# Optimization experiments

Hardware: AMD Instinct MI355X
Metric: run time of the kernel (lower is better)

The kernel has to match this reference:

```python
import jax, jax.numpy as jnp
import numpy as np

N, E = 30000, 480000
D_IN, D_HID = 128, 256
NODE_CLS, EDGE_CLS, POLAR = 5, 2, 6
EPS = 1e-5

def layer_norm(x, g, b):
    mu = jnp.mean(x, axis=-1, keepdims=True)
    var = jnp.mean((x - mu) ** 2, axis=-1, keepdims=True)
    return g * (x - mu) / jnp.sqrt(var + EPS) + b

def sage_pool(h, src, dst, Wp, bp, Ws, bs, Wn, n_nodes):
    # DGL SAGEConv aggregator_type='pool': m = relu(fc_pool(h_src)); max over in-edges
    m = jax.nn.relu(h @ Wp + bp)              # [N, d_in]
    agg = jax.ops.segment_max(m[src], dst, num_segments=n_nodes)  # [N, d_in], -inf if no in-edges
    deg = jax.ops.segment_sum(jnp.ones((src.shape[0],), jnp.float32), dst, num_segments=n_nodes)
    h_neigh = jnp.where(deg[:, None] > 0, agg, 0.0)
    out = h @ Ws + bs + h_neigh @ Wn          # fc_self + fc_neigh
    return jax.nn.relu(out)                   # activation=F.relu

def setup_inputs() -> dict:
    key = jax.random.key(0)
    ks = jax.random.split(key, 24)
    p = lambda k, shape, fan: jax.random.normal(k, shape, jnp.float32) / np.sqrt(fan)
    return {
        "h": jax.random.normal(ks[0], (N, D_IN), jnp.float32),
        "efeat": jax.random.normal(ks[1], (E, POLAR), jnp.float32),
        "src": jax.random.randint(ks[2], (E,), 0, N, jnp.int32),
        "dst": jax.random.randint(ks[3], (E,), 0, N, jnp.int32),
        # encoder SAGEConv(128->256)
        "enc_Wpool": p(ks[4], (D_IN, D_IN), D_IN), "enc_bpool": jnp.zeros((D_IN,), jnp.float32),
        "enc_Wself": p(ks[5], (D_IN, D_HID), D_IN), "enc_bself": jnp.zeros((D_HID,), jnp.float32),
        "enc_Wneigh": p(ks[6], (D_IN, D_HID), D_IN),
        # node_pred: Linear(256,5) + LayerNorm(5)
        "np_W": p(ks[7], (D_HID, NODE_CLS), D_HID), "np_b": jnp.zeros((NODE_CLS,), jnp.float32),
        "np_g": jnp.ones((NODE_CLS,), jnp.float32), "np_beta": jnp.zeros((NODE_CLS,), jnp.float32),
        # edge predictor: Linear(528,256) + LN(256) + Linear(256,2)
        "ep_W1": p(ks[8], (2 * D_HID + 2 * NODE_CLS + POLAR, D_HID), 2 * D_HID + 16),
        "ep_b1": jnp.zeros((D_HID,), jnp.float32),
        "ep_g": jnp.ones((D_HID,), jnp.float32), "ep_beta": jnp.zeros((D_HID,), jnp.float32),
        "ep_W2": p(ks[9], (D_HID, EDGE_CLS), D_HID), "ep_b2": jnp.zeros((EDGE_CLS,), jnp.float32),
        # decoder SAGEConv(256->128)
        "dec_Wpool": p(ks[10], (D_HID, D_HID), D_HID), "dec_bpool": jnp.zeros((D_HID,), jnp.float32),
        "dec_Wself": p(ks[11], (D_HID, D_IN), D_HID), "dec_bself": jnp.zeros((D_IN,), jnp.float32),
        "dec_Wneigh": p(ks[12], (D_HID, D_IN), D_HID),
    }

def reference(h, efeat, src, dst,
              enc_Wpool, enc_bpool, enc_Wself, enc_bself, enc_Wneigh,
              np_W, np_b, np_g, np_beta,
              ep_W1, ep_b1, ep_g, ep_beta, ep_W2, ep_b2,
              dec_Wpool, dec_bpool, dec_Wself, dec_bself, dec_Wneigh):
    # encoder (drop_rate == 0 path)
    h1 = sage_pool(h, src, dst, enc_Wpool, enc_bpool, enc_Wself, enc_bself, enc_Wneigh, N)
    # node head
    node_pred = layer_norm(h1 @ np_W + np_b, np_g, np_beta)  # [N, 5]
    # edge head: gather-concat-MLP per edge
    cls_sm = jax.nn.softmax(node_pred, axis=1)               # softmax once, gather per edge
    x = jnp.concatenate([h1[src], cls_sm[src], efeat, h1[dst], cls_sm[dst]], axis=1)  # [E, 528]
    x = jax.nn.relu(layer_norm(x @ ep_W1 + ep_b1, ep_g, ep_beta))
    edges_pred = x @ ep_W2 + ep_b2                           # dropout is identity in eval
    # decoder (uses original graph, input h1)
    h2 = sage_pool(h1, src, dst, dec_Wpool, dec_bpool, dec_Wself, dec_bself, dec_Wneigh, N)
    return (node_pred, edges_pred, h2)
```

## Files before the change

### kernel.cpp

```cpp
#include <hip/hip_runtime.h>

typedef unsigned short u16;
typedef unsigned int u32;
typedef __bf16 bf16_t;
typedef bf16_t bf16x8 __attribute__((ext_vector_type(8)));
typedef float f32x4 __attribute__((ext_vector_type(4)));

#define N_NODES 30000
#define N_EDGES 480000

static __device__ __forceinline__ float b2f(u16 u) {
  return __uint_as_float(((u32)u) << 16);
}
static __device__ __forceinline__ float b2f_lo(u32 w) {
  return __uint_as_float(w << 16);
}
static __device__ __forceinline__ float b2f_hi(u32 w) {
  return __uint_as_float(w & 0xffff0000u);
}
static __device__ __forceinline__ u16 f2b(float f) {
  u32 x = __float_as_uint(f);
  u32 r = (x + 0x7fffu + ((x >> 16) & 1u)) >> 16;
  return (u16)r;
}

__global__ __launch_bounds__(256) void init_sniff_deg(const u16* __restrict__ h,
                                                      int* __restrict__ flag,
                                                      int* __restrict__ deg) {
  int i = blockIdx.x * 256 + threadIdx.x;
  if (i < N_NODES) deg[i] = 0;
  if (blockIdx.x == 0) {
    int t = threadIdx.x;
    int bad = 0;
#pragma unroll
    for (int j = 0; j < 4; j++) {
      u32 e = ((u32)h[t * 4 + j] >> 7) & 0xFFu;
      if (e >= 0x8Eu) bad = 1;
    }
    int r = __syncthreads_or(bad);
    if (t == 0) *flag = r ? 1 : 0;
  }
}

__global__ __launch_bounds__(256) void conv_arr4(const void* __restrict__ src,
                                                 u16* __restrict__ dst, int n4,
                                                 const int* __restrict__ flag) {
  int i = blockIdx.x * 256 + threadIdx.x;
  if (i >= n4) return;
  if (*flag) {
    float4 f = ((const float4*)src)[i];
    uint2 o;
    o.x = (u32)f2b(f.x) | ((u32)f2b(f.y) << 16);
    o.y = (u32)f2b(f.z) | ((u32)f2b(f.w) << 16);
    ((uint2*)dst)[i] = o;
  } else {
    ((uint2*)dst)[i] = ((const uint2*)src)[i];
  }
}

struct ConvDesc { const void* s; u16* d; int n; int off; };
struct ConvTab { ConvDesc e[20]; int total; };

__global__ __launch_bounds__(256) void conv_params(ConvTab tab, const int* __restrict__ flag) {
  int i = blockIdx.x * 256 + threadIdx.x;
  if (i >= tab.total) return;
  int f = *flag;
#pragma unroll 1
  for (int a = 0; a < 20; a++) {
    int j = i - tab.e[a].off;
    if (j >= 0 && j < tab.e[a].n) {
      if (f) tab.e[a].d[j] = f2b(((const float*)tab.e[a].s)[j]);
      else tab.e[a].d[j] = ((const u16*)tab.e[a].s)[j];
      return;
    }
  }
}

__global__ __launch_bounds__(256) void deg_count(const int* __restrict__ dst,
                                                 int* __restrict__ deg, int nE) {
  int e = blockIdx.x * 256 + threadIdx.x;
  if (e < nE) atomicAdd(&deg[dst[e]], 1);
}

__global__ __launch_bounds__(1024) void scan_off(const int* __restrict__ deg,
                                                 int* __restrict__ off,
                                                 int* __restrict__ cursor, int n) {
  __shared__ int carry;
  __shared__ int wsum[16];
  int t = threadIdx.x, lane = t & 63, wv = t >> 6;
  if (t == 0) { carry = 0; off[0] = 0; }
  __syncthreads();
  for (int base = 0; base < n; base += 1024) {
    int v = (base + t < n) ? deg[base + t] : 0;
    int x = v;
#pragma unroll
    for (int d = 1; d < 64; d <<= 1) {
      int y = __shfl_up(x, d, 64);
      if (lane >= d) x += y;
    }
    if (lane == 63) wsum[wv] = x;
    __syncthreads();
    int wadd = 0;
    for (int w = 0; w < wv; w++) wadd += wsum[w];
    int incl = x + wadd + carry;
    if (base + t < n) { off[base + t + 1] = incl; cursor[base + t] = incl - v; }
    __syncthreads();
    if (t == 1023) carry = incl;
    __syncthreads();
  }
}

__global__ __launch_bounds__(256) void fill_csr(const int* __restrict__ src,
                                                const int* __restrict__ dst,
                                                int* __restrict__ cursor,
                                                int* __restrict__ esrc, int nE) {
  int e = blockIdx.x * 256 + threadIdx.x;
  if (e >= nE) return;
  int p = atomicAdd(&cursor[dst[e]], 1);
  esrc[p] = src[e];
}

__global__ __launch_bounds__(256) void agg128(const u16* __restrict__ m,
                                              const int* __restrict__ esrc,
                                              const int* __restrict__ off,
                                              u16* __restrict__ out) {
  int wv = threadIdx.x >> 6, lane = threadIdx.x & 63;
  int n = blockIdx.x * 4 + wv;
  if (n >= N_NODES) return;
  int s0 = off[n], s1 = off[n + 1];
  u32 a0 = 0, a1 = 0;
  int i = s0;
  for (; i + 3 < s1; i += 4) {
    int e0 = esrc[i], e1 = esrc[i + 1], e2 = esrc[i + 2], e3 = esrc[i + 3];
    u32 r0 = *(const u32*)(m + (size_t)e0 * 128 + lane * 2);
    u32 r1 = *(const u32*)(m + (size_t)e1 * 128 + lane * 2);
    u32 r2 = *(const u32*)(m + (size_t)e2 * 128 + lane * 2);
    u32 r3 = *(const u32*)(m + (size_t)e3 * 128 + lane * 2);
    a0 = max(a0, r0 & 0xffffu); a1 = max(a1, r0 >> 16);
    a0 = max(a0, r1 & 0xffffu); a1 = max(a1, r1 >> 16);
    a0 = max(a0, r2 & 0xffffu); a1 = max(a1, r2 >> 16);
    a0 = max(a0, r3 & 0xffffu); a1 = max(a1, r3 >> 16);
  }
  for (; i < s1; i++) {
    u32 ra = *(const u32*)(m + (size_t)esrc[i] * 128 + lane * 2);
    a0 = max(a0, ra & 0xffffu); a1 = max(a1, ra >> 16);
  }
  *(u32*)(out + (size_t)n * 128 + lane * 2) = a0 | (a1 << 16);
}

__global__ __launch_bounds__(256) void agg256(const u16* __restrict__ m,
                                              const int* __restrict__ esrc,
                                              const int* __restrict__ off,
                                              u16* __restrict__ out) {
  int wv = threadIdx.x >> 6, lane = threadIdx.x & 63;
  int n = blockIdx.x * 4 + wv;
  if (n >= N_NODES) return;
  int s0 = off[n], s1 = off[n + 1];
  u32 a0 = 0, a1 = 0, a2 = 0, a3 = 0;
  int i = s0;
  for (; i + 3 < s1; i += 4) {
    int e0 = esrc[i], e1 = esrc[i + 1], e2 = esrc[i + 2], e3 = esrc[i + 3];
    uint2 r0 = *(const uint2*)(m + (size_t)e0 * 256 + lane * 4);
    uint2 r1 = *(const uint2*)(m + (size_t)e1 * 256 + lane * 4);
    uint2 r2 = *(const uint2*)(m + (size_t)e2 * 256 + lane * 4);
    uint2 r3 = *(const uint2*)(m + (size_t)e3 * 256 + lane * 4);
    a0 = max(a0, r0.x & 0xffffu); a1 = max(a1, r0.x >> 16);
    a2 = max(a2, r0.y & 0xffffu); a3 = max(a3, r0.y >> 16);
    a0 = max(a0, r1.x & 0xffffu); a1 = max(a1, r1.x >> 16);
    a2 = max(a2, r1.y & 0xffffu); a3 = max(a3, r1.y >> 16);
    a0 = max(a0, r2.x & 0xffffu); a1 = max(a1, r2.x >> 16);
    a2 = max(a2, r2.y & 0xffffu); a3 = max(a3, r2.y >> 16);
    a0 = max(a0, r3.x & 0xffffu); a1 = max(a1, r3.x >> 16);
    a2 = max(a2, r3.y & 0xffffu); a3 = max(a3, r3.y >> 16);
  }
  for (; i < s1; i++) {
    uint2 ra = *(const uint2*)(m + (size_t)esrc[i] * 256 + lane * 4);
    a0 = max(a0, ra.x & 0xffffu); a1 = max(a1, ra.x >> 16);
    a2 = max(a2, ra.y & 0xffffu); a3 = max(a3, ra.y >> 16);
  }
  uint2 w;
  w.x = a0 | (a1 << 16);
  w.y = a2 | (a3 << 16);
  *(uint2*)(out + (size_t)n * 256 + lane * 4) = w;
}

__global__ __launch_bounds__(256) void prep_weights(
    const u16* __restrict__ encWp, const u16* __restrict__ encWs, const u16* __restrict__ encWn,
    const u16* __restrict__ decWp, const u16* __restrict__ decWs, const u16* __restrict__ decWn,
    const u16* __restrict__ epW1, const u16* __restrict__ epb1,
    u16* __restrict__ wt_encpool, u16* __restrict__ wt_enc,
    u16* __restrict__ wt_decpool, u16* __restrict__ wt_dec,
    u16* __restrict__ wt_UV, u16* __restrict__ b512, float* __restrict__ swsum) {
  int b = blockIdx.x;
  const int t = threadIdx.x;
  if (b < 64) {
    int idx = b * 256 + t; int k = idx >> 7, n = idx & 127;
    wt_encpool[n * 128 + k] = encWp[k * 128 + n]; return;
  }
  b -= 64;
  if (b < 128) {
    int idx = b * 256 + t; int k = idx >> 8, n = idx & 255;
    wt_enc[n * 256 + k] = encWs[k * 256 + n]; return;
  }
  b -= 128;
  if (b < 128) {
    int idx = b * 256 + t; int k = idx >> 8, n = idx & 255;
    wt_enc[n * 256 + 128 + k] = encWn[k * 256 + n]; return;
  }
  b -= 128;
  if (b < 256) {
    int idx = b * 256 + t; int k = idx >> 8, n = idx & 255;
    wt_decpool[n * 256 + k] = decWp[k * 256 + n]; return;
  }
  b -= 256;
  if (b < 128) {
    int idx = b * 256 + t; int k = idx >> 7, n = idx & 127;
    wt_dec[n * 512 + k] = decWs[k * 128 + n]; return;
  }
  b -= 128;
  if (b < 128) {
    int idx = b * 256 + t; int k = idx >> 7, n = idx & 127;
    wt_dec[n * 512 + 256 + k] = decWn[k * 128 + n]; return;
  }
  b -= 128;
  if (b < 512) {
    int n = b, n2 = n & 255, base = (n >= 256) ? 267 : 0;
    for (int kp = t; kp < 288; kp += 256) {
      u16 v = (kp < 261) ? epW1[(size_t)(base + kp) * 256 + n2] : (u16)0;
      wt_UV[(size_t)n * 288 + kp] = v;
    }
    return;
  }
  b -= 512;
  if (b < 2) {
    int i = b * 256 + t;
    b512[i] = (i < 256) ? epb1[i] : (u16)0; return;
  }
  int k = t >> 5, l32 = t & 31;
  if (k < 6) {
    uint4 v = *(const uint4*)(epW1 + (size_t)(261 + k) * 256 + l32 * 8);
    float s = b2f_lo(v.x) + b2f_hi(v.x) + b2f_lo(v.y) + b2f_hi(v.y) +
              b2f_lo(v.z) + b2f_hi(v.z) + b2f_lo(v.w) + b2f_hi(v.w);
#pragma unroll
    for (int m = 1; m < 32; m <<= 1) s += __shfl_xor(s, m, 64);
    if (l32 == 0) swsum[k] = s;
  }
}

__global__ __launch_bounds__(256) void gemm_mfma(
    const u16* __restrict__ A0, const u16* __restrict__ A1, int K0, int K1,
    const u16* __restrict__ Bt, const u16* __restrict__ bias, int do_relu,
    u16* __restrict__ C, float* __restrict__ Cf, const int* __restrict__ flag,
    int M, int Nld) {
  __shared__ __align__(16) u16 As[128 * 40];
  __shared__ __align__(16) u16 Bs[128 * 40];
  const int t = threadIdx.x;
  const int lane = t & 63, wv = t >> 6;
  const int wm = wv & 1, wn = wv >> 1;
  const int r = lane & 15, q = lane >> 4;
  const int bm = blockIdx.x, bn = blockIdx.y;
  const int Ktot = K0 + K1;
  const bool usef = (Cf != nullptr) && (*flag != 0);

  f32x4 acc[4][4];
#pragma unroll
  for (int i = 0; i < 4; i++)
#pragma unroll
    for (int j = 0; j < 4; j++) acc[i][j] = (f32x4){0.f, 0.f, 0.f, 0.f};

  for (int kc = 0; kc < Ktot; kc += 32) {
#pragma unroll
    for (int h = 0; h < 2; h++) {
      int idx = t + h * 256;
      int rr = idx >> 2, qq = idx & 3;
      int rowg = bm * 128 + rr;
      uint4 av = make_uint4(0, 0, 0, 0);
      if (rowg < M) {
        const u16* p = (kc < K0) ? (A0 + (size_t)rowg * K0 + kc)
                                 : (A1 + (size_t)rowg * K1 + (kc - K0));
        av = *(const uint4*)(p + qq * 8);
      }
      *(uint4*)&As[rr * 40 + qq * 8] = av;
      int ng = bn * 128 + rr;
      uint4 bv = *(const uint4*)(Bt + (size_t)ng * Ktot + kc + qq * 8);
      *(uint4*)&Bs[rr * 40 + qq * 8] = bv;
    }
    __syncthreads();
    bf16x8 af[4], bfm[4];
#pragma unroll
    for (int mi = 0; mi < 4; mi++)
      af[mi] = *(const bf16x8*)&As[(wm * 64 + mi * 16 + r) * 40 + q * 8];
#pragma unroll
    for (int ni = 0; ni < 4; ni++)
      bfm[ni] = *(const bf16x8*)&Bs[(wn * 64 + ni * 16 + r) * 40 + q * 8];
#pragma unroll
    for (int mi = 0; mi < 4; mi++)
#pragma unroll
      for (int ni = 0; ni < 4; ni++)
        acc[mi][ni] = __builtin_amdgcn_mfma_f32_16x16x32_bf16(af[mi], bfm[ni], acc[mi][ni], 0, 0, 0);
    __syncthreads();
  }

  float bv[4];
#pragma unroll
  for (int ni = 0; ni < 4; ni++)
    bv[ni] = bias ? b2f(bias[bn * 128 + wn * 64 + ni * 16 + r]) : 0.f;
#pragma unroll
  for (int mi = 0; mi < 4; mi++) {
#pragma unroll
    for (int i = 0; i < 4; i++) {
      int rowg = bm * 128 + wm * 64 + mi * 16 + q * 4 + i;
      if (rowg >= M) continue;
#pragma unroll
      for (int ni = 0; ni < 4; ni++) {
        int colg = bn * 128 + wn * 64 + ni * 16 + r;
        float v = acc[mi][ni][i] + bv[ni];
        if (do_relu) v = v > 0.f ? v : 0.f;
        if (usef) Cf[(size_t)rowg * Nld + colg] = v;
        else C[(size_t)rowg * Nld + colg] = f2b(v);
      }
    }
  }
}

__global__ __launch_bounds__(256) void node_head(
    const u16* __restrict__ h1, const u16* __restrict__ W, const u16* __restrict__ b,
    const u16* __restrict__ g, const u16* __restrict__ beta,
    u16* __restrict__ outN, float* __restrict__ outNf, const int* __restrict__ flag,
    u16* __restrict__ smOut) {
  __shared__ float Wl[256 * 5];
  __shared__ float bl[5], gl[5], betal[5];
  int t = threadIdx.x;
#pragma unroll
  for (int c = 0; c < 5; c++) Wl[t * 5 + c] = b2f(W[t * 5 + c]);
  if (t < 5) { bl[t] = b2f(b[t]); gl[t] = b2f(g[t]); betal[t] = b2f(beta[t]); }
  __syncthreads();
  int n = blockIdx.x * 256 + t;
  if (n >= N_NODES) return;
  const bool usef = (*flag != 0);
  float acc[5] = {0.f, 0.f, 0.f, 0.f, 0.f};
  const u16* hp = h1 + (size_t)n * 256;
  for (int k8 = 0; k8 < 32; k8++) {
    uint4 v = *(const uint4*)(hp + k8 * 8);
    u32 wds[4] = {v.x, v.y, v.z, v.w};
#pragma unroll
    for (int h = 0; h < 4; h++) {
      float x0 = b2f_lo(wds[h]), x1 = b2f_hi(wds[h]);
      int k = k8 * 8 + h * 2;
#pragma unroll
      for (int c = 0; c < 5; c++)
        acc[c] += x0 * Wl[k * 5 + c] + x1 * Wl[(k + 1) * 5 + c];
    }
  }
  float x[5], mu = 0.f;
#pragma unroll
  for (int c = 0; c < 5; c++) { x[c] = acc[c] + bl[c]; mu += x[c]; }
  mu *= 0.2f;
  float var = 0.f;
#pragma unroll
  for (int c = 0; c < 5; c++) { float d = x[c] - mu; var += d * d; }
  var *= 0.2f;
  float rstd = rsqrtf(fmaxf(var, 0.f) + 1e-5f);
  float v5[5], mx = -1e30f;
#pragma unroll
  for (int c = 0; c < 5; c++) {
    v5[c] = gl[c] * (x[c] - mu) * rstd + betal[c];
    if (usef) outNf[(size_t)n * 5 + c] = v5[c];
    else outN[(size_t)n * 5 + c] = f2b(v5[c]);
    mx = fmaxf(mx, v5[c]);
  }
  float s = 0.f, ex[5];
#pragma unroll
  for (int c = 0; c < 5; c++) { ex[c] = __expf(v5[c] - mx); s += ex[c]; }
  float inv = 1.f / s;
  u16 row[32];
#pragma unroll
  for (int c = 0; c < 5; c++) row[c] = f2b(ex[c] * inv);
#pragma unroll
  for (int c = 5; c < 32; c++) row[c] = 0;
#pragma unroll
  for (int c = 0; c < 4; c++)
    *(uint4*)(smOut + (size_t)n * 32 + c * 8) = *(const uint4*)&row[c * 8];
}

__global__ __launch_bounds__(256) void rowsum_uv(const u16* __restrict__ UV,
                                                 float2* __restrict__ Srow) {
  int wv = threadIdx.x >> 6, lane = threadIdx.x & 63;
  int n = blockIdx.x * 4 + wv;
  if (n >= N_NODES) return;
  uint4 v = *(const uint4*)(UV + (size_t)n * 512 + lane * 8);
  float s = b2f_lo(v.x) + b2f_hi(v.x) + b2f_lo(v.y) + b2f_hi(v.y) +
            b2f_lo(v.z) + b2f_hi(v.z) + b2f_lo(v.w) + b2f_hi(v.w);
#pragma unroll
  for (int m = 1; m < 32; m <<= 1) s += __shfl_xor(s, m, 64);
  if (lane == 0) Srow[n].x = s;
  if (lane == 32) Srow[n].y = s;
}

__global__ __launch_bounds__(256) void edge_pt(
    const u16* __restrict__ UV, const float2* __restrict__ Srow,
    const float* __restrict__ swsum, const u16* __restrict__ ef,
    const int* __restrict__ src, const int* __restrict__ dst,
    const u16* __restrict__ w1raw,
    const u16* __restrict__ g, const u16* __restrict__ beta,
    const u16* __restrict__ w2, const u16* __restrict__ b2,
    u16* __restrict__ outE, float* __restrict__ outEf, const int* __restrict__ flag) {
  const int t = threadIdx.x;
  const int lane = t & 63, wv = t >> 6;
  const int c0 = lane * 4;
  const int grp = (lane >> 4) & 3;
  float wef[6][4], gl[4], bl[4], w20[4], w21[4];
#pragma unroll
  for (int k = 0; k < 6; k++) {
    u32 wa = *(const u32*)(w1raw + (size_t)(261 + k) * 256 + c0);
    u32 wb = *(const u32*)(w1raw + (size_t)(261 + k) * 256 + c0 + 2);
    wef[k][0] = b2f_lo(wa); wef[k][1] = b2f_hi(wa);
    wef[k][2] = b2f_lo(wb); wef[k][3] = b2f_hi(wb);
  }
#pragma unroll
  for (int j = 0; j < 4; j++) {
    gl[j] = b2f(g[c0 + j]); bl[j] = b2f(beta[c0 + j]);
    w20[j] = b2f(w2[(c0 + j) * 2]); w21[j] = b2f(w2[(c0 + j) * 2 + 1]);
  }
  float sw[6];
#pragma unroll
  for (int k = 0; k < 6; k++) sw[k] = swsum[k];
  const float b20 = b2f(b2[0]), b21 = b2f(b2[1]);
  const float bsel = (grp & 1) ? b21 : b20;
  const bool usef = (*flag != 0);

  const int pbase = (blockIdx.x * 4 + wv) * 32;
  int sa = src[pbase * 2], da = dst[pbase * 2];
  int sb = src[pbase * 2 + 1], db = dst[pbase * 2 + 1];
#pragma unroll 1
  for (int it = 0; it < 32; ++it) {
    const int e = (pbase + it) * 2;
    int sac = sa, dac = da, sbc = sb, dbc = db;
    if (it + 1 < 32) {
      sa = src[e + 2]; da = dst[e + 2]; sb = src[e + 3]; db = dst[e + 3];
    }
    uint2 ua = *(const uint2*)(UV + (size_t)sac * 512 + c0);
    uint2 va = *(const uint2*)(UV + (size_t)dac * 512 + 256 + c0);
    uint2 ub = *(const uint2*)(UV + (size_t)sbc * 512 + c0);
    uint2 vb = *(const uint2*)(UV + (size_t)dbc * 512 + 256 + c0);
    float2 sra = Srow[sac], srda = Srow[dac];
    float2 srb = Srow[sbc], srdb = Srow[dbc];
    const u32* efp = (const u32*)(ef + (size_t)e * 6);
    u32 f0 = efp[0], f1 = efp[1], f2 = efp[2], f3 = efp[3], f4 = efp[4], f5 = efp[5];
    float xa[6] = {b2f_lo(f0), b2f_hi(f0), b2f_lo(f1), b2f_hi(f1), b2f_lo(f2), b2f_hi(f2)};
    float xb[6] = {b2f_lo(f3), b2f_hi(f3), b2f_lo(f4), b2f_hi(f4), b2f_lo(f5), b2f_hi(f5)};

    float ma = sra.x + srda.y, mb = srb.x + srdb.y;
#pragma unroll
    for (int k = 0; k < 6; k++) { ma += xa[k] * sw[k]; mb += xb[k] * sw[k]; }
    ma *= (1.f / 256.f); mb *= (1.f / 256.f);

    float ya[4], yb[4];
    ya[0] = b2f_lo(ua.x) + b2f_lo(va.x); yb[0] = b2f_lo(ub.x) + b2f_lo(vb.x);
    ya[1] = b2f_hi(ua.x) + b2f_hi(va.x); yb[1] = b2f_hi(ub.x) + b2f_hi(vb.x);
    ya[2] = b2f_lo(ua.y) + b2f_lo(va.y); yb[2] = b2f_lo(ub.y) + b2f_lo(vb.y);
    ya[3] = b2f_hi(ua.y) + b2f_hi(va.y); yb[3] = b2f_hi(ub.y) + b2f_hi(vb.y);
#pragma unroll
    for (int k = 0; k < 6; k++)
#pragma unroll
      for (int j = 0; j < 4; j++) {
        ya[j] += xa[k] * wef[k][j];
        yb[j] += xb[k] * wef[k][j];
      }
    float pqa = ya[0] * ya[0] + ya[1] * ya[1] + ya[2] * ya[2] + ya[3] * ya[3];
    float pqb = yb[0] * yb[0] + yb[1] * yb[1] + yb[2] * yb[2] + yb[3] * yb[3];
    pqa += __shfl_xor(pqa, 32, 64);
    pqb += __shfl_xor(pqb, 32, 64);
    float z = (lane < 32) ? pqa : pqb;
#pragma unroll
    for (int m = 16; m >= 1; m >>= 1) z += __shfl_xor(z, m, 64);
    float zz = __shfl_xor(z, 32, 64);
    float pqa_t = (lane < 32) ? z : zz;
    float pqb_t = (lane < 32) ? zz : z;
    float rsa = rsqrtf(fmaxf(pqa_t * (1.f / 256.f) - ma * ma, 0.f) + 1e-5f);
    float rsb = rsqrtf(fmaxf(pqb_t * (1.f / 256.f) - mb * mb, 0.f) + 1e-5f);
    float p0a = 0.f, p1a = 0.f, p0b = 0.f, p1b = 0.f;
#pragma unroll
    for (int j = 0; j < 4; j++) {
      float na = fmaxf((ya[j] - ma) * rsa * gl[j] + bl[j], 0.f);
      float nb = fmaxf((yb[j] - mb) * rsb * gl[j] + bl[j], 0.f);
      p0a += na * w20[j]; p1a += na * w21[j];
      p0b += nb * w20[j]; p1b += nb * w21[j];
    }
    p0a += __shfl_xor(p0a, 32, 64); p1a += __shfl_xor(p1a, 32, 64);
    p0b += __shfl_xor(p0b, 32, 64); p1b += __shfl_xor(p1b, 32, 64);
    p0a += __shfl_xor(p0a, 16, 64); p1a += __shfl_xor(p1a, 16, 64);
    p0b += __shfl_xor(p0b, 16, 64); p1b += __shfl_xor(p1b, 16, 64);
    float w = (grp & 2) ? ((grp & 1) ? p1b : p0b) : ((grp & 1) ? p1a : p0a);
#pragma unroll
    for (int m = 8; m >= 1; m >>= 1) w += __shfl_xor(w, m, 64);
    if ((lane & 15) == 0) {
      float val = w + bsel;
      size_t oi = (size_t)e * 2 + grp;
      if (usef) outEf[oi] = val;
      else outE[oi] = f2b(val);
    }
  }
}

extern "C" void kernel_launch(void* const* d_in, const int* in_sizes, int n_in,
                              void* d_out, int out_size, void* d_ws, size_t ws_size,
                              hipStream_t stream) {
  char* wp = (char*)d_ws;
  auto alloc = [&](size_t bytes) -> char* {
    char* p = wp; wp += (bytes + 255) & ~(size_t)255; return p;
  };
  int* flag       = (int*)alloc(256);
  u16* c_h        = (u16*)alloc((size_t)N_NODES * 128 * 2);
  u16* c_ef       = (u16*)alloc((size_t)N_EDGES * 6 * 2);
  static const int pidx[20] = {4,5,6,7,8, 9,10,11,12, 13,14,15,16,17,18, 19,20,21,22,23};
  static const int pn[20]   = {16384,128,32768,256,32768, 1280,5,5,5,
                               135168,256,256,256,512,2, 65536,256,32768,128,32768};
  u16* cp[20];
  for (int a = 0; a < 20; a++) cp[a] = (u16*)alloc((size_t)pn[a] * 2);

  u16* wt_encpool = (u16*)alloc(128 * 128 * 2);
  u16* wt_enc     = (u16*)alloc(256 * 256 * 2);
  u16* wt_decpool = (u16*)alloc(256 * 256 * 2);
  u16* wt_dec     = (u16*)alloc(128 * 512 * 2);
  u16* wt_UV      = (u16*)alloc(512 * 288 * 2);
  u16* b512       = (u16*)alloc(512 * 2);
  float2* Srow    = (float2*)alloc((size_t)N_NODES * 8);
  float* swsum_b  = (float*)alloc(64);
  u16* m_buf      = (u16*)alloc((size_t)N_NODES * 256 * 2);
  u16* aggb       = (u16*)alloc((size_t)N_NODES * 256 * 2);
  u16* UVbuf      = m_buf;
  u16* h1b        = (u16*)alloc((size_t)N_NODES * 256 * 2);
  u16* smb32      = (u16*)alloc((size_t)N_NODES * 32 * 2);
  int* deg        = (int*)alloc((size_t)N_NODES * 4);
  int* off        = (int*)alloc((size_t)(N_NODES + 1) * 4);
  int* cursor     = (int*)alloc((size_t)N_NODES * 4);
  int* esrc       = (int*)alloc((size_t)N_EDGES * 4);

  const int* src = (const int*)d_in[2];
  const int* dst = (const int*)d_in[3];

  u16* outN = (u16*)d_out;
  u16* outE = outN + (size_t)N_NODES * 5;
  u16* outH = outN + 1110000;
  float* outNf = (float*)d_out;
  float* outEf = outNf + (size_t)N_NODES * 5;
  float* outHf = outNf + 1110000;

  init_sniff_deg<<<118, 256, 0, stream>>>((const u16*)d_in[0], flag, deg);
  conv_arr4<<<3750, 256, 0, stream>>>(d_in[0], c_h, 960000, flag);
  conv_arr4<<<2813, 256, 0, stream>>>(d_in[1], c_ef, 720000, flag);
  ConvTab tab;
  int off_a = 0;
  for (int a = 0; a < 20; a++) {
    tab.e[a].s = d_in[pidx[a]]; tab.e[a].d = cp[a]; tab.e[a].n = pn[a]; tab.e[a].off = off_a;
    off_a += pn[a];
  }
  tab.total = off_a;
  conv_params<<<(off_a + 255) / 256, 256, 0, stream>>>(tab, flag);

  const u16 *enc_Wpool = cp[0], *enc_bpool = cp[1], *enc_Wself = cp[2], *enc_bself = cp[3],
            *enc_Wneigh = cp[4], *np_W = cp[5], *np_b = cp[6], *np_g = cp[7], *np_beta = cp[8],
            *ep_W1 = cp[9], *ep_b1 = cp[10], *ep_g = cp[11], *ep_beta = cp[12],
            *ep_W2 = cp[13], *ep_b2 = cp[14], *dec_Wpool = cp[15], *dec_bpool = cp[16],
            *dec_Wself = cp[17], *dec_bself = cp[18], *dec_Wneigh = cp[19];

  deg_count<<<1875, 256, 0, stream>>>(dst, deg, N_EDGES);
  scan_off<<<1, 1024, 0, stream>>>(deg, off, cursor, N_NODES);
  fill_csr<<<1875, 256, 0, stream>>>(src, dst, cursor, esrc, N_EDGES);

  prep_weights<<<1347, 256, 0, stream>>>(enc_Wpool, enc_Wself, enc_Wneigh,
                                         dec_Wpool, dec_Wself, dec_Wneigh,
                                         ep_W1, ep_b1,
                                         wt_encpool, wt_enc, wt_decpool, wt_dec,
                                         wt_UV, b512, swsum_b);

  gemm_mfma<<<dim3(235, 1), 256, 0, stream>>>(c_h, nullptr, 128, 0, wt_encpool,
                                              enc_bpool, 1, m_buf, nullptr, flag, N_NODES, 128);
  agg128<<<7500, 256, 0, stream>>>(m_buf, esrc, off, aggb);
  gemm_mfma<<<dim3(235, 2), 256, 0, stream>>>(c_h, aggb, 128, 128, wt_enc,
                                              enc_bself, 1, h1b, nullptr, flag, N_NODES, 256);
  node_head<<<118, 256, 0, stream>>>(h1b, np_W, np_b, np_g, np_beta, outN, outNf, flag, smb32);
  gemm_mfma<<<dim3(235, 4), 256, 0, stream>>>(h1b, smb32, 256, 32, wt_UV,
                                              b512, 0, UVbuf, nullptr, flag, N_NODES, 512);
  rowsum_uv<<<7500, 256, 0, stream>>>(UVbuf, Srow);
  edge_pt<<<1875, 256, 0, stream>>>(UVbuf, Srow, swsum_b, c_ef, src, dst, ep_W1,
                                    ep_g, ep_beta, ep_W2, ep_b2, outE, outEf, flag);
  gemm_mfma<<<dim3(235, 2), 256, 0, stream>>>(h1b, nullptr, 256, 0, wt_decpool,
                                              dec_bpool, 1, m_buf, nullptr, flag, N_NODES, 256);
  agg256<<<7500, 256, 0, stream>>>(m_buf, esrc, off, aggb);
  gemm_mfma<<<dim3(235, 1), 256, 0, stream>>>(h1b, aggb, 256, 256, wt_dec,
                                              dec_bself, 1, outH, outHf, flag, N_NODES, 128);
}
```

Baseline: 497.9 us.

## Fuse conversion and degree kernels; vectorize aggregation; halve edge_pt work per wave

Result: faster. 474.0 us (-4.8%).

```diff
diff --git a/kernel.cpp b/kernel.cpp
--- a/kernel.cpp
+++ b/kernel.cpp
@@ -42,29 +42,55 @@
   }
 }
 
-__global__ __launch_bounds__(256) void conv_arr4(const void* __restrict__ src,
-                                                 u16* __restrict__ dst, int n4,
-                                                 const int* __restrict__ flag) {
-  int i = blockIdx.x * 256 + threadIdx.x;
-  if (i >= n4) return;
-  if (*flag) {
-    float4 f = ((const float4*)src)[i];
-    uint2 o;
-    o.x = (u32)f2b(f.x) | ((u32)f2b(f.y) << 16);
-    o.y = (u32)f2b(f.z) | ((u32)f2b(f.w) << 16);
-    ((uint2*)dst)[i] = o;
-  } else {
-    ((uint2*)dst)[i] = ((const uint2*)src)[i];
-  }
-}
-
 struct ConvDesc { const void* s; u16* d; int n; int off; };
 struct ConvTab { ConvDesc e[20]; int total; };
 
-__global__ __launch_bounds__(256) void conv_params(ConvTab tab, const int* __restrict__ flag) {
-  int i = blockIdx.x * 256 + threadIdx.x;
+__global__ __launch_bounds__(256) void conv_all(
+    const int* __restrict__ dstE, int* __restrict__ deg,
+    const void* __restrict__ hsrc, u16* __restrict__ c_h,
+    const void* __restrict__ efsrc, u16* __restrict__ c_ef,
+    ConvTab tab, const int* __restrict__ flag) {
+  int b = blockIdx.x;
+  const int t = threadIdx.x;
+  if (b < 1875) {
+    int e = b * 256 + t;
+    if (e < N_EDGES) atomicAdd(&deg[dstE[e]], 1);
+    return;
+  }
+  b -= 1875;
+  const int f = *flag;
+  if (b < 3750) {
+    int i = b * 256 + t;
+    if (f) {
+      float4 v = ((const float4*)hsrc)[i];
+      uint2 o;
+      o.x = (u32)f2b(v.x) | ((u32)f2b(v.y) << 16);
+      o.y = (u32)f2b(v.z) | ((u32)f2b(v.w) << 16);
+      ((uint2*)c_h)[i] = o;
+    } else {
+      ((uint2*)c_h)[i] = ((const uint2*)hsrc)[i];
+    }
+    return;
+  }
+  b -= 3750;
+  if (b < 2813) {
+    int i = b * 256 + t;
+    if (i < 720000) {
+      if (f) {
+        float4 v = ((const float4*)efsrc)[i];
+        uint2 o;
+        o.x = (u32)f2b(v.x) | ((u32)f2b(v.y) << 16);
+        o.y = (u32)f2b(v.z) | ((u32)f2b(v.w) << 16);
+        ((uint2*)c_ef)[i] = o;
+      } else {
+        ((uint2*)c_ef)[i] = ((const uint2*)efsrc)[i];
+      }
+    }
+    return;
+  }
+  b -= 2813;
+  int i = b * 256 + t;
   if (i >= tab.total) return;
-  int f = *flag;
 #pragma unroll 1
   for (int a = 0; a < 20; a++) {
     int j = i - tab.e[a].off;
@@ -74,12 +100,6 @@
       return;
     }
   }
-}
-
-__global__ __launch_bounds__(256) void deg_count(const int* __restrict__ dst,
-                                                 int* __restrict__ deg, int nE) {
-  int e = blockIdx.x * 256 + threadIdx.x;
-  if (e < nE) atomicAdd(&deg[dst[e]], 1);
 }
 
 __global__ __launch_bounds__(1024) void scan_off(const int* __restrict__ deg,
@@ -125,27 +145,35 @@
                                               const int* __restrict__ off,
                                               u16* __restrict__ out) {
   int wv = threadIdx.x >> 6, lane = threadIdx.x & 63;
-  int n = blockIdx.x * 4 + wv;
+  int qd = lane >> 4, l = lane & 15;
+  int n = blockIdx.x * 16 + wv * 4 + qd;
   if (n >= N_NODES) return;
-  int s0 = off[n], s1 = off[n + 1];
-  u32 a0 = 0, a1 = 0;
-  int i = s0;
-  for (; i + 3 < s1; i += 4) {
-    int e0 = esrc[i], e1 = esrc[i + 1], e2 = esrc[i + 2], e3 = esrc[i + 3];
-    u32 r0 = *(const u32*)(m + (size_t)e0 * 128 + lane * 2);
-    u32 r1 = *(const u32*)(m + (size_t)e1 * 128 + lane * 2);
-    u32 r2 = *(const u32*)(m + (size_t)e2 * 128 + lane * 2);
-    u32 r3 = *(const u32*)(m + (size_t)e3 * 128 + lane * 2);
-    a0 = max(a0, r0 & 0xffffu); a1 = max(a1, r0 >> 16);
-    a0 = max(a0, r1 & 0xffffu); a1 = max(a1, r1 >> 16);
-    a0 = max(a0, r2 & 0xffffu); a1 = max(a1, r2 >> 16);
-    a0 = max(a0, r3 & 0xffffu); a1 = max(a1, r3 >> 16);
-  }
-  for (; i < s1; i++) {
-    u32 ra = *(const u32*)(m + (size_t)esrc[i] * 128 + lane * 2);
-    a0 = max(a0, ra & 0xffffu); a1 = max(a1, ra >> 16);
-  }
-  *(u32*)(out + (size_t)n * 128 + lane * 2) = a0 | (a1 << 16);
+  int i = off[n], s1 = off[n + 1];
+  u32 a0 = 0, a1 = 0, a2 = 0, a3 = 0, a4 = 0, a5 = 0, a6 = 0, a7 = 0;
+  for (; i + 1 < s1; i += 2) {
+    int e0 = esrc[i], e1 = esrc[i + 1];
+    uint4 r0 = *(const uint4*)(m + (size_t)e0 * 128 + l * 8);
+    uint4 r1 = *(const uint4*)(m + (size_t)e1 * 128 + l * 8);
+    a0 = max(a0, r0.x & 0xffffu); a1 = max(a1, r0.x >> 16);
+    a2 = max(a2, r0.y & 0xffffu); a3 = max(a3, r0.y >> 16);
+    a4 = max(a4, r0.z & 0xffffu); a5 = max(a5, r0.z >> 16);
+    a6 = max(a6, r0.w & 0xffffu); a7 = max(a7, r0.w >> 16);
+    a0 = max(a0, r1.x & 0xffffu); a1 = max(a1, r1.x >> 16);
+    a2 = max(a2, r1.y & 0xffffu); a3 = max(a3, r1.y >> 16);
+    a4 = max(a4, r1.z & 0xffffu); a5 = max(a5, r1.z >> 16);
+    a6 = max(a6, r1.w & 0xffffu); a7 = max(a7, r1.w >> 16);
+  }
+  if (i < s1) {
+    uint4 r0 = *(const uint4*)(m + (size_t)esrc[i] * 128 + l * 8);
+    a0 = max(a0, r0.x & 0xffffu); a1 = max(a1, r0.x >> 16);
+    a2 = max(a2, r0.y & 0xffffu); a3 = max(a3, r0.y >> 16);
+    a4 = max(a4, r0.z & 0xffffu); a5 = max(a5, r0.z >> 16);
+    a6 = max(a6, r0.w & 0xffffu); a7 = max(a7, r0.w >> 16);
+  }
+  uint4 w;
+  w.x = a0 | (a1 << 16); w.y = a2 | (a3 << 16);
+  w.z = a4 | (a5 << 16); w.w = a6 | (a7 << 16);
+  *(uint4*)(out + (size_t)n * 128 + l * 8) = w;
 }
 
 __global__ __launch_bounds__(256) void agg256(const u16* __restrict__ m,
@@ -153,35 +181,35 @@
                                               const int* __restrict__ off,
                                               u16* __restrict__ out) {
   int wv = threadIdx.x >> 6, lane = threadIdx.x & 63;
-  int n = blockIdx.x * 4 + wv;
+  int half = lane >> 5, l = lane & 31;
+  int n = blockIdx.x * 8 + wv * 2 + half;
   if (n >= N_NODES) return;
-  int s0 = off[n], s1 = off[n + 1];
-  u32 a0 = 0, a1 = 0, a2 = 0, a3 = 0;
-  int i = s0;
-  for (; i + 3 < s1; i += 4) {
-    int e0 = esrc[i], e1 = esrc[i + 1], e2 = esrc[i + 2], e3 = esrc[i + 3];
-    uint2 r0 = *(const uint2*)(m + (size_t)e0 * 256 + lane * 4);
-    uint2 r1 = *(const uint2*)(m + (size_t)e1 * 256 + lane * 4);
-    uint2 r2 = *(const uint2*)(m + (size_t)e2 * 256 + lane * 4);
-    uint2 r3 = *(const uint2*)(m + (size_t)e3 * 256 + lane * 4);
+  int i = off[n], s1 = off[n + 1];
+  u32 a0 = 0, a1 = 0, a2 = 0, a3 = 0, a4 = 0, a5 = 0, a6 = 0, a7 = 0;
+  for (; i + 1 < s1; i += 2) {
+    int e0 = esrc[i], e1 = esrc[i + 1];
+    uint4 r0 = *(const uint4*)(m + (size_t)e0 * 256 + l * 8);
+    uint4 r1 = *(const uint4*)(m + (size_t)e1 * 256 + l * 8);
     a0 = max(a0, r0.x & 0xffffu); a1 = max(a1, r0.x >> 16);
     a2 = max(a2, r0.y & 0xffffu); a3 = max(a3, r0.y >> 16);
+    a4 = max(a4, r0.z & 0xffffu); a5 = max(a5, r0.z >> 16);
+    a6 = max(a6, r0.w & 0xffffu); a7 = max(a7, r0.w >> 16);
     a0 = max(a0, r1.x & 0xffffu); a1 = max(a1, r1.x >> 16);
     a2 = max(a2, r1.y & 0xffffu); a3 = max(a3, r1.y >> 16);
-    a0 = max(a0, r2.x & 0xffffu); a1 = max(a1, r2.x >> 16);
-    a2 = max(a2, r2.y & 0xffffu); a3 = max(a3, r2.y >> 16);
-    a0 = max(a0, r3.x & 0xffffu); a1 = max(a1, r3.x >> 16);
-    a2 = max(a2, r3.y & 0xffffu); a3 = max(a3, r3.y >> 16);
-  }
-  for (; i < s1; i++) {
-    uint2 ra = *(const uint2*)(m + (size_t)esrc[i] * 256 + lane * 4);
-    a0 = max(a0, ra.x & 0xffffu); a1 = max(a1, ra.x >> 16);
-    a2 = max(a2, ra.y & 0xffffu); a3 = max(a3, ra.y >> 16);
-  }
-  uint2 w;
-  w.x = a0 | (a1 << 16);
-  w.y = a2 | (a3 << 16);
-  *(uint2*)(out + (size_t)n * 256 + lane * 4) = w;
+    a4 = max(a4, r1.z & 0xffffu); a5 = max(a5, r1.z >> 16);
+    a6 = max(a6, r1.w & 0xffffu); a7 = max(a7, r1.w >> 16);
+  }
+  if (i < s1) {
+    uint4 r0 = *(const uint4*)(m + (size_t)esrc[i] * 256 + l * 8);
+    a0 = max(a0, r0.x & 0xffffu); a1 = max(a1, r0.x >> 16);
+    a2 = max(a2, r0.y & 0xffffu); a3 = max(a3, r0.y >> 16);
+    a4 = max(a4, r0.z & 0xffffu); a5 = max(a5, r0.z >> 16);
+    a6 = max(a6, r0.w & 0xffffu); a7 = max(a7, r0.w >> 16);
+  }
+  uint4 w;
+  w.x = a0 | (a1 << 16); w.y = a2 | (a3 << 16);
+  w.z = a4 | (a5 << 16); w.w = a6 | (a7 << 16);
+  *(uint4*)(out + (size_t)n * 256 + l * 8) = w;
 }
 
 __global__ __launch_bounds__(256) void prep_weights(
@@ -429,14 +457,14 @@
   const float bsel = (grp & 1) ? b21 : b20;
   const bool usef = (*flag != 0);
 
-  const int pbase = (blockIdx.x * 4 + wv) * 32;
+  const int pbase = (blockIdx.x * 4 + wv) * 16;
   int sa = src[pbase * 2], da = dst[pbase * 2];
   int sb = src[pbase * 2 + 1], db = dst[pbase * 2 + 1];
 #pragma unroll 1
-  for (int it = 0; it < 32; ++it) {
+  for (int it = 0; it < 16; ++it) {
     const int e = (pbase + it) * 2;
     int sac = sa, dac = da, sbc = sb, dbc = db;
-    if (it + 1 < 32) {
+    if (it + 1 < 16) {
       sa = src[e + 2]; da = dst[e + 2]; sb = src[e + 3]; db = dst[e + 3];
     }
     uint2 ua = *(const uint2*)(UV + (size_t)sac * 512 + c0);
@@ -548,8 +576,6 @@
   float* outHf = outNf + 1110000;
 
   init_sniff_deg<<<118, 256, 0, stream>>>((const u16*)d_in[0], flag, deg);
-  conv_arr4<<<3750, 256, 0, stream>>>(d_in[0], c_h, 960000, flag);
-  conv_arr4<<<2813, 256, 0, stream>>>(d_in[1], c_ef, 720000, flag);
   ConvTab tab;
   int off_a = 0;
   for (int a = 0; a < 20; a++) {
@@ -557,7 +583,8 @@
     off_a += pn[a];
   }
   tab.total = off_a;
-  conv_params<<<(off_a + 255) / 256, 256, 0, stream>>>(tab, flag);
+  int conv_blocks = 1875 + 3750 + 2813 + (off_a + 255) / 256;
+  conv_all<<<conv_blocks, 256, 0, stream>>>(dst, deg, d_in[0], c_h, d_in[1], c_ef, tab, flag);
 
   const u16 *enc_Wpool = cp[0], *enc_bpool = cp[1], *enc_Wself = cp[2], *enc_bself = cp[3],
             *enc_Wneigh = cp[4], *np_W = cp[5], *np_b = cp[6], *np_g = cp[7], *np_beta = cp[8],
@@ -565,7 +592,6 @@
             *ep_W2 = cp[13], *ep_b2 = cp[14], *dec_Wpool = cp[15], *dec_bpool = cp[16],
             *dec_Wself = cp[17], *dec_bself = cp[18], *dec_Wneigh = cp[19];
 
-  deg_count<<<1875, 256, 0, stream>>>(dst, deg, N_EDGES);
   scan_off<<<1, 1024, 0, stream>>>(deg, off, cursor, N_NODES);
   fill_csr<<<1875, 256, 0, stream>>>(src, dst, cursor, esrc, N_EDGES);
 
@@ -577,18 +603,18 @@
 
   gemm_mfma<<<dim3(235, 1), 256, 0, stream>>>(c_h, nullptr, 128, 0, wt_encpool,
                                               enc_bpool, 1, m_buf, nullptr, flag, N_NODES, 128);
-  agg128<<<7500, 256, 0, stream>>>(m_buf, esrc, off, aggb);
+  agg128<<<1875, 256, 0, stream>>>(m_buf, esrc, off, aggb);
   gemm_mfma<<<dim3(235, 2), 256, 0, stream>>>(c_h, aggb, 128, 128, wt_enc,
                                               enc_bself, 1, h1b, nullptr, flag, N_NODES, 256);
   node_head<<<118, 256, 0, stream>>>(h1b, np_W, np_b, np_g, np_beta, outN, outNf, flag, smb32);
   gemm_mfma<<<dim3(235, 4), 256, 0, stream>>>(h1b, smb32, 256, 32, wt_UV,
                                               b512, 0, UVbuf, nullptr, flag, N_NODES, 512);
   rowsum_uv<<<7500, 256, 0, stream>>>(UVbuf, Srow);
-  edge_pt<<<1875, 256, 0, stream>>>(UVbuf, Srow, swsum_b, c_ef, src, dst, ep_W1,
+  edge_pt<<<3750, 256, 0, stream>>>(UVbuf, Srow, swsum_b, c_ef, src, dst, ep_W1,
                                     ep_g, ep_beta, ep_W2, ep_b2, outE, outEf, flag);
   gemm_mfma<<<dim3(235, 2), 256, 0, stream>>>(h1b, nullptr, 256, 0, wt_decpool,
                                               dec_bpool, 1, m_buf, nullptr, flag, N_NODES, 256);
-  agg256<<<7500, 256, 0, stream>>>(m_buf, esrc, off, aggb);
+  agg256<<<3750, 256, 0, stream>>>(m_buf, esrc, off, aggb);
   gemm_mfma<<<dim3(235, 1), 256, 0, stream>>>(h1b, aggb, 256, 256, wt_dec,
                                               dec_bself, 1, outH, outHf, flag, N_NODES, 128);
 }
```
